# Kernel optimization log

Measured on AMD Instinct MI355X. Metric: run time of the kernel, lower is better.

The kernel has to match this reference:

```python
import jax, jax.numpy as jnp
import numpy as np

N, V, C, H, W, P = 4, 5, 128, 128, 128, 4096
IMG_W, IMG_H = 1920.0, 1080.0
FM = 128.0


def setup_inputs() -> dict:
    key = jax.random.key(0)
    k1, k2, k3, k4 = jax.random.split(key, 4)
    feature_maps = jax.random.normal(k1, (N, V, C, H, W), jnp.float32)
    xy = jax.random.uniform(k2, (N, P, 2), jnp.float32, -800.0, 800.0)
    z = jax.random.uniform(k3, (N, P, 1), jnp.float32, 100.0, 2000.0)
    extra = jax.random.uniform(k4, (N, P, 2), jnp.float32)
    sample_points = jnp.concatenate([xy, z, extra], axis=-1)  # [N,P,5]
    R = jnp.tile(jnp.eye(3, dtype=jnp.float32), (N, V, 1, 1))
    T = jnp.tile(jnp.array([0.0, 0.0, -3000.0], jnp.float32), (N, V, 1))
    f = jnp.full((N, V, 2), 1200.0, jnp.float32)
    c = jnp.tile(jnp.array([IMG_W / 2, IMG_H / 2], jnp.float32), (N, V, 1))
    k = jnp.zeros((N, V, 3), jnp.float32)  # radial distortion
    p = jnp.zeros((N, V, 2), jnp.float32)  # tangential distortion
    # affine transform (from get_affine_transform): full image -> feature map
    trans = jnp.tile(jnp.array([[FM / IMG_W, 0.0, 0.0], [0.0, FM / IMG_H, 0.0]], jnp.float32), (N, V, 1, 1))
    wh = jnp.tile(jnp.array([IMG_W, IMG_H], jnp.float32), (N, V, 1))
    fm_size = jnp.array([FM, FM], jnp.float32)
    return dict(feature_maps=feature_maps, sample_points=sample_points, R=R, T=T,
                f=f, c=c, k=k, p=p, trans=trans, wh=wh, fm_size=fm_size)


def _grid_sample_one(img, grid):
    # img: [C,H,W], grid: [P,2] in normalized coords; bilinear, zeros padding, align_corners=True
    Ci, Hi, Wi = img.shape
    x = (grid[:, 0] + 1.0) * 0.5 * (Wi - 1)
    y = (grid[:, 1] + 1.0) * 0.5 * (Hi - 1)
    x0 = jnp.floor(x); y0 = jnp.floor(y)
    wx1 = x - x0; wx0 = 1.0 - wx1
    wy1 = y - y0; wy0 = 1.0 - wy1

    def gather(xi, yi):
        valid = (xi >= 0) & (xi <= Wi - 1) & (yi >= 0) & (yi <= Hi - 1)
        xc = jnp.clip(xi, 0, Wi - 1).astype(jnp.int32)
        yc = jnp.clip(yi, 0, Hi - 1).astype(jnp.int32)
        return img[:, yc, xc] * valid.astype(img.dtype)  # [C,P]

    return (gather(x0, y0) * (wx0 * wy0) + gather(x0 + 1, y0) * (wx1 * wy0)
            + gather(x0, y0 + 1) * (wx0 * wy1) + gather(x0 + 1, y0 + 1) * (wx1 * wy1))


def _forward(feature_maps, sample_points, R, T, f, c, k, p, trans, wh, fm_size):
    n, v, ch, h, w = feature_maps.shape
    pts = sample_points[:, :, :3]  # [N,P,3]
    # world -> camera: X_cam = R @ (X - T)
    Xc = jnp.einsum('nvij,nvpj->nvpi', R, pts[:, None, :, :] - T[:, :, None, :])  # [N,V,P,3]
    xn = Xc[..., 0] / Xc[..., 2]
    yn = Xc[..., 1] / Xc[..., 2]
    r2 = xn * xn + yn * yn
    k1 = k[..., 0:1]; k2 = k[..., 1:2]; k3 = k[..., 2:3]
    p1 = p[..., 0:1]; p2 = p[..., 1:2]
    radial = 1.0 + k1 * r2 + k2 * r2 * r2 + k3 * r2 * r2 * r2
    xd = xn * radial + 2.0 * p1 * xn * yn + p2 * (r2 + 2.0 * xn * xn)
    yd = yn * radial + p1 * (r2 + 2.0 * yn * yn) + 2.0 * p2 * xn * yn
    xy = jnp.stack([xd, yd], -1) * f[:, :, None, :] + c[:, :, None, :]  # [N,V,P,2] pixel coords
    width = wh[..., 0:1]; height = wh[..., 1:2]
    bound = ((xy[..., 0] >= 0) & (xy[..., 1] >= 0)
             & (xy[..., 0] < width) & (xy[..., 1] < height)).astype(feature_maps.dtype)  # [N,V,P]
    max_wh = jnp.maximum(wh[..., 0], wh[..., 1])[:, :, None, None]
    pix = jnp.clip(xy, -1.0, max_wh)
    # affine transform to feature-map coords
    pix_t = jnp.einsum('nvij,nvpj->nvpi', trans[..., :2], pix) + trans[..., 2][:, :, None, :]
    norm = jnp.clip(pix_t / (fm_size - 1.0) * 2.0 - 1.0, -1.1, 1.1)  # [N,V,P,2]
    sampled = jax.vmap(_grid_sample_one)(feature_maps.reshape(n * v, ch, h, w),
                                         norm.reshape(n * v, -1, 2))  # [NV,C,P]
    sampled = sampled.reshape(n, v, ch, -1)
    feats = (sampled * bound[:, :, None, :]).transpose(0, 3, 1, 2)  # [N,P,V,C]
    is_not_nan = jnp.logical_not(jnp.isnan(feats).any(axis=(2, 3)))  # [N,P]
    bounding = (bound.sum(axis=1) > 0) & is_not_nan  # discard_nan=False path
    return feats, bounding


def reference(feature_maps, sample_points, R, T, f, c, k, p, trans, wh, fm_size):
    feats, bounding = _forward(feature_maps, sample_points, R, T, f, c, k, p, trans, wh, fm_size)
    return feats, bounding, sample_points
```

## Files before the change

### kernel.cpp

```cpp
#include <hip/hip_runtime.h>
#include <math.h>

#define N 4
#define V 5
#define C 128
#define H 128
#define W 128
#define P 4096
#define HW (H * W)
#define PTS 16

typedef float  fvec4 __attribute__((ext_vector_type(4)));
typedef unsigned short usvec4 __attribute__((ext_vector_type(4)));

__device__ __forceinline__ unsigned short f2bf_rne(float x) {
    unsigned u = __float_as_uint(x);
    unsigned rounding = 0x7fffu + ((u >> 16) & 1u);
    return (unsigned short)((u + rounding) >> 16);
}
__device__ __forceinline__ float bf2f(unsigned short b) {
    return __uint_as_float(((unsigned)b) << 16);
}

__global__ __launch_bounds__(256) void transpose_kernel(
    const float* __restrict__ fm, unsigned short* __restrict__ fmT)
{
    const int nv  = blockIdx.y;
    const int hw0 = blockIdx.x * 64;
    __shared__ float lds[64][C + 1];

    const int t = threadIdx.x;

    {
        const int hwl = (t & 15) * 4;
        const int cb  = t >> 4;
        const float* src = fm + (size_t)nv * C * HW + hw0 + hwl;
        for (int c = cb; c < C; c += 16) {
            const fvec4 v = __builtin_nontemporal_load(
                (const fvec4*)(src + (size_t)c * HW));
            lds[hwl + 0][c] = v.x;
            lds[hwl + 1][c] = v.y;
            lds[hwl + 2][c] = v.z;
            lds[hwl + 3][c] = v.w;
        }
    }
    __syncthreads();

    {
        const int c4 = (t & 31) * 4;
        unsigned short* dst = fmT + ((size_t)nv * HW + hw0) * C + c4;
        for (int hw = (t >> 5); hw < 64; hw += 8) {
            const fvec4 v = *(const fvec4*)&lds[hw][c4];
            usvec4 o;
            o.x = f2bf_rne(v.x);
            o.y = f2bf_rne(v.y);
            o.z = f2bf_rne(v.z);
            o.w = f2bf_rne(v.w);
            *(usvec4*)(dst + (size_t)hw * C) = o;
        }
    }
}

__global__ __launch_bounds__(256) void project_sample_kernel(
    const unsigned short* __restrict__ fmT,
    const float* __restrict__ sp,
    const float* __restrict__ Rm,
    const float* __restrict__ Tm,
    const float* __restrict__ fv,
    const float* __restrict__ cv,
    const float* __restrict__ kv,
    const float* __restrict__ pv,
    const float* __restrict__ trans,
    const float* __restrict__ wh,
    const float* __restrict__ fmsz,
    float* __restrict__ out_feats,
    float* __restrict__ out_bound,
    float* __restrict__ out_sp)
{
    const int pb = blockIdx.x;
    const int n  = pb >> 8;
    const int p0 = (pb & 255) * PTS;
    const int t  = threadIdx.x;
    const int base_pt = n * P + p0;

    __shared__ int   s_idx[PTS * V][4];
    __shared__ float s_w[PTS * V][4];
    __shared__ float s_bnd[PTS * V];
    __shared__ int   s_nan[PTS];

    if (t < PTS) s_nan[t] = 0;
    if (t < PTS * 5) out_sp[base_pt * 5 + t] = sp[base_pt * 5 + t];

    if (t < PTS * V) {
        const int pt = t / V;
        const int v  = t - pt * V;
        const int nv = n * V + v;

        const float X = sp[(base_pt + pt) * 5 + 0];
        const float Y = sp[(base_pt + pt) * 5 + 1];
        const float Z = sp[(base_pt + pt) * 5 + 2];

        const float* Rv = Rm + nv * 9;
        const float tx = Tm[nv * 3 + 0], ty = Tm[nv * 3 + 1], tz = Tm[nv * 3 + 2];
        const float px = X - tx, py = Y - ty, pz = Z - tz;
        const float Xc0 = Rv[0] * px + Rv[1] * py + Rv[2] * pz;
        const float Xc1 = Rv[3] * px + Rv[4] * py + Rv[5] * pz;
        const float Xc2 = Rv[6] * px + Rv[7] * py + Rv[8] * pz;
        const float xn = Xc0 / Xc2;
        const float yn = Xc1 / Xc2;
        const float r2 = xn * xn + yn * yn;
        const float k1 = kv[nv * 3 + 0], k2 = kv[nv * 3 + 1], k3 = kv[nv * 3 + 2];
        const float p1 = pv[nv * 2 + 0], p2 = pv[nv * 2 + 1];
        const float radial = 1.0f + k1 * r2 + k2 * r2 * r2 + k3 * r2 * r2 * r2;
        const float xd = xn * radial + 2.0f * p1 * xn * yn + p2 * (r2 + 2.0f * xn * xn);
        const float yd = yn * radial + p1 * (r2 + 2.0f * yn * yn) + 2.0f * p2 * xn * yn;
        const float xy0 = xd * fv[nv * 2 + 0] + cv[nv * 2 + 0];
        const float xy1 = yd * fv[nv * 2 + 1] + cv[nv * 2 + 1];
        const float width  = wh[nv * 2 + 0];
        const float height = wh[nv * 2 + 1];
        const bool bound = (xy0 >= 0.0f) && (xy1 >= 0.0f) && (xy0 < width) && (xy1 < height);
        const float maxwh = fmaxf(width, height);
        const float pix0 = fminf(fmaxf(xy0, -1.0f), maxwh);
        const float pix1 = fminf(fmaxf(xy1, -1.0f), maxwh);
        const float* tr = trans + nv * 6;
        const float pt0 = tr[0] * pix0 + tr[1] * pix1 + tr[2];
        const float pt1 = tr[3] * pix0 + tr[4] * pix1 + tr[5];
        const float fm0 = fmsz[0], fm1 = fmsz[1];
        float g0 = pt0 / (fm0 - 1.0f) * 2.0f - 1.0f;
        float g1 = pt1 / (fm1 - 1.0f) * 2.0f - 1.0f;
        g0 = fminf(fmaxf(g0, -1.1f), 1.1f);
        g1 = fminf(fmaxf(g1, -1.1f), 1.1f);

        const float xg = (g0 + 1.0f) * 0.5f * (float)(W - 1);
        const float yg = (g1 + 1.0f) * 0.5f * (float)(H - 1);
        const float x0f = floorf(xg), y0f = floorf(yg);
        const float wx1 = xg - x0f, wx0 = 1.0f - wx1;
        const float wy1 = yg - y0f, wy0 = 1.0f - wy1;
        const int x0 = (int)x0f, y0 = (int)y0f;
        const int x1 = x0 + 1,  y1 = y0 + 1;
        const bool vx0 = (x0 >= 0) && (x0 <= W - 1);
        const bool vx1 = (x1 >= 0) && (x1 <= W - 1);
        const bool vy0 = (y0 >= 0) && (y0 <= H - 1);
        const bool vy1 = (y1 >= 0) && (y1 <= H - 1);
        const int x0c = min(max(x0, 0), W - 1);
        const int x1c = min(max(x1, 0), W - 1);
        const int y0c = min(max(y0, 0), H - 1);
        const int y1c = min(max(y1, 0), H - 1);

        s_idx[t][0] = y0c * W + x0c;
        s_idx[t][1] = y0c * W + x1c;
        s_idx[t][2] = y1c * W + x0c;
        s_idx[t][3] = y1c * W + x1c;
        s_w[t][0] = (vx0 && vy0) ? (wx0 * wy0) : 0.0f;
        s_w[t][1] = (vx1 && vy0) ? (wx1 * wy0) : 0.0f;
        s_w[t][2] = (vx0 && vy1) ? (wx0 * wy1) : 0.0f;
        s_w[t][3] = (vx1 && vy1) ? (wx1 * wy1) : 0.0f;
        s_bnd[t] = bound ? 1.0f : 0.0f;
    }
    __syncthreads();

    {
        const int grp = t >> 5;
        const int c4  = (t & 31) * 4;
        const unsigned short* img_n = fmT + (size_t)(n * V) * HW * C;
        #pragma unroll 2
        for (int i = grp; i < PTS * V; i += 8) {
            const int pt = i / V;
            const int v  = i - pt * V;
            const unsigned short* img = img_n + (size_t)v * HW * C + c4;
            const usvec4 b00 = *(const usvec4*)(img + (size_t)s_idx[i][0] * C);
            const usvec4 b10 = *(const usvec4*)(img + (size_t)s_idx[i][1] * C);
            const usvec4 b01 = *(const usvec4*)(img + (size_t)s_idx[i][2] * C);
            const usvec4 b11 = *(const usvec4*)(img + (size_t)s_idx[i][3] * C);
            const float w00 = s_w[i][0], w10 = s_w[i][1];
            const float w01 = s_w[i][2], w11 = s_w[i][3];
            const float bnd = s_bnd[i];
            fvec4 f;
            f.x = (bf2f(b00.x) * w00 + bf2f(b10.x) * w10
                 + bf2f(b01.x) * w01 + bf2f(b11.x) * w11) * bnd;
            f.y = (bf2f(b00.y) * w00 + bf2f(b10.y) * w10
                 + bf2f(b01.y) * w01 + bf2f(b11.y) * w11) * bnd;
            f.z = (bf2f(b00.z) * w00 + bf2f(b10.z) * w10
                 + bf2f(b01.z) * w01 + bf2f(b11.z) * w11) * bnd;
            f.w = (bf2f(b00.w) * w00 + bf2f(b10.w) * w10
                 + bf2f(b01.w) * w01 + bf2f(b11.w) * w11) * bnd;
            if ((f.x != f.x) | (f.y != f.y) | (f.z != f.z) | (f.w != f.w))
                s_nan[pt] = 1;
            __builtin_nontemporal_store(
                f, (fvec4*)&out_feats[((size_t)(base_pt + pt) * V + v) * C + c4]);
        }
    }
    __syncthreads();

    if (t < PTS) {
        bool any_b = false;
        #pragma unroll
        for (int v = 0; v < V; ++v) any_b |= (s_bnd[t * V + v] != 0.0f);
        out_bound[base_pt + t] = (any_b && (s_nan[t] == 0)) ? 1.0f : 0.0f;
    }
}

extern "C" void kernel_launch(void* const* d_in, const int* in_sizes, int n_in,
                              void* d_out, int out_size, void* d_ws, size_t ws_size,
                              hipStream_t stream) {
    const float* fm    = (const float*)d_in[0];
    const float* sp    = (const float*)d_in[1];
    const float* Rm    = (const float*)d_in[2];
    const float* Tm    = (const float*)d_in[3];
    const float* fv    = (const float*)d_in[4];
    const float* cv    = (const float*)d_in[5];
    const float* kv    = (const float*)d_in[6];
    const float* pv    = (const float*)d_in[7];
    const float* trans = (const float*)d_in[8];
    const float* wh    = (const float*)d_in[9];
    const float* fmsz  = (const float*)d_in[10];

    float* out        = (float*)d_out;
    float* out_feats  = out;
    float* out_bound  = out + (size_t)N * P * V * C;
    float* out_sp     = out_bound + (size_t)N * P;

    unsigned short* fmT = (unsigned short*)d_ws;

    dim3 tgrid(HW / 64, N * V);
    transpose_kernel<<<tgrid, 256, 0, stream>>>(fm, fmT);

    project_sample_kernel<<<N * (P / PTS), 256, 0, stream>>>(
        fmT, sp, Rm, Tm, fv, cv, kv, pv, trans, wh, fmsz,
        out_feats, out_bound, out_sp);
}
```

Measured before the change: 287.2 us.

## Transpose only feature-map tiles touched by projected sample points

Projection moves into its own kernel. It writes per-sample corner indices and weights to workspace and marks which 16x16 tiles of each view's feature map are referenced. The transpose-to-bf16 kernel then converts only the flagged tiles, and the gather kernel reads the precomputed records. This aims to avoid reading and converting the whole fp32 feature map when samples cover only part of it, at the cost of less coalesced tile loads and an extra launch. Flags are never cleared, so stale flags from earlier calls can cause extra tile work.

```diff
diff --git a/kernel.cpp b/kernel.cpp
--- a/kernel.cpp
+++ b/kernel.cpp
@@ -9,6 +9,7 @@
 #define P 4096
 #define HW (H * W)
 #define PTS 16
+#define NPV (N * P * V)
 
 typedef float  fvec4 __attribute__((ext_vector_type(4)));
 typedef unsigned short usvec4 __attribute__((ext_vector_type(4)));
@@ -22,66 +23,153 @@
     return __uint_as_float(((unsigned)b) << 16);
 }
 
-__global__ __launch_bounds__(256) void transpose_kernel(
-    const float* __restrict__ fm, unsigned short* __restrict__ fmT)
+__global__ __launch_bounds__(256) void project_kernel(
+    const float* __restrict__ sp,
+    const float* __restrict__ Rm, const float* __restrict__ Tm,
+    const float* __restrict__ fv, const float* __restrict__ cv,
+    const float* __restrict__ kv, const float* __restrict__ pv,
+    const float* __restrict__ trans, const float* __restrict__ wh,
+    const float* __restrict__ fmsz,
+    int4*  __restrict__ ws_idx,
+    float4* __restrict__ ws_w,
+    float* __restrict__ ws_bnd,
+    unsigned* __restrict__ flags,
+    float* __restrict__ out_sp)
 {
-    const int nv  = blockIdx.y;
-    const int hw0 = blockIdx.x * 64;
-    __shared__ float lds[64][C + 1];
-
+    const int tid = blockIdx.x * 256 + threadIdx.x;
+    out_sp[tid] = sp[tid];
+
+    const int pt = tid / V;
+    const int v  = tid - pt * V;
+    const int n  = pt >> 12;
+    const int nv = n * V + v;
+
+    const float X = sp[pt * 5 + 0];
+    const float Y = sp[pt * 5 + 1];
+    const float Z = sp[pt * 5 + 2];
+
+    const float* Rv = Rm + nv * 9;
+    const float tx = Tm[nv * 3 + 0], ty = Tm[nv * 3 + 1], tz = Tm[nv * 3 + 2];
+    const float px = X - tx, py = Y - ty, pz = Z - tz;
+    const float Xc0 = Rv[0] * px + Rv[1] * py + Rv[2] * pz;
+    const float Xc1 = Rv[3] * px + Rv[4] * py + Rv[5] * pz;
+    const float Xc2 = Rv[6] * px + Rv[7] * py + Rv[8] * pz;
+    const float xn = Xc0 / Xc2;
+    const float yn = Xc1 / Xc2;
+    const float r2 = xn * xn + yn * yn;
+    const float k1 = kv[nv * 3 + 0], k2 = kv[nv * 3 + 1], k3 = kv[nv * 3 + 2];
+    const float p1 = pv[nv * 2 + 0], p2 = pv[nv * 2 + 1];
+    const float radial = 1.0f + k1 * r2 + k2 * r2 * r2 + k3 * r2 * r2 * r2;
+    const float xd = xn * radial + 2.0f * p1 * xn * yn + p2 * (r2 + 2.0f * xn * xn);
+    const float yd = yn * radial + p1 * (r2 + 2.0f * yn * yn) + 2.0f * p2 * xn * yn;
+    const float xy0 = xd * fv[nv * 2 + 0] + cv[nv * 2 + 0];
+    const float xy1 = yd * fv[nv * 2 + 1] + cv[nv * 2 + 1];
+    const float width  = wh[nv * 2 + 0];
+    const float height = wh[nv * 2 + 1];
+    const bool bound = (xy0 >= 0.0f) && (xy1 >= 0.0f) && (xy0 < width) && (xy1 < height);
+    const float maxwh = fmaxf(width, height);
+    const float pix0 = fminf(fmaxf(xy0, -1.0f), maxwh);
+    const float pix1 = fminf(fmaxf(xy1, -1.0f), maxwh);
+    const float* tr = trans + nv * 6;
+    const float pt0 = tr[0] * pix0 + tr[1] * pix1 + tr[2];
+    const float pt1 = tr[3] * pix0 + tr[4] * pix1 + tr[5];
+    const float fm0 = fmsz[0], fm1 = fmsz[1];
+    float g0 = pt0 / (fm0 - 1.0f) * 2.0f - 1.0f;
+    float g1 = pt1 / (fm1 - 1.0f) * 2.0f - 1.0f;
+    g0 = fminf(fmaxf(g0, -1.1f), 1.1f);
+    g1 = fminf(fmaxf(g1, -1.1f), 1.1f);
+
+    const float xg = (g0 + 1.0f) * 0.5f * (float)(W - 1);
+    const float yg = (g1 + 1.0f) * 0.5f * (float)(H - 1);
+    const float x0f = floorf(xg), y0f = floorf(yg);
+    const float wx1 = xg - x0f, wx0 = 1.0f - wx1;
+    const float wy1 = yg - y0f, wy0 = 1.0f - wy1;
+    const int x0 = (int)x0f, y0 = (int)y0f;
+    const int x1 = x0 + 1,  y1 = y0 + 1;
+    const bool vx0 = (x0 >= 0) && (x0 <= W - 1);
+    const bool vx1 = (x1 >= 0) && (x1 <= W - 1);
+    const bool vy0 = (y0 >= 0) && (y0 <= H - 1);
+    const bool vy1 = (y1 >= 0) && (y1 <= H - 1);
+    const int x0c = min(max(x0, 0), W - 1);
+    const int x1c = min(max(x1, 0), W - 1);
+    const int y0c = min(max(y0, 0), H - 1);
+    const int y1c = min(max(y1, 0), H - 1);
+
+    int4 id;
+    id.x = y0c * W + x0c;
+    id.y = y0c * W + x1c;
+    id.z = y1c * W + x0c;
+    id.w = y1c * W + x1c;
+    ws_idx[tid] = id;
+
+    float4 w;
+    w.x = (vx0 && vy0) ? (wx0 * wy0) : 0.0f;
+    w.y = (vx1 && vy0) ? (wx1 * wy0) : 0.0f;
+    w.z = (vx0 && vy1) ? (wx0 * wy1) : 0.0f;
+    w.w = (vx1 && vy1) ? (wx1 * wy1) : 0.0f;
+    ws_w[tid] = w;
+    ws_bnd[tid] = bound ? 1.0f : 0.0f;
+
+    unsigned* fl = flags + nv * 64;
+    const int tx0 = x0c >> 4, tx1 = x1c >> 4;
+    const int ty0 = y0c >> 4, ty1 = y1c >> 4;
+    fl[ty0 * 8 + tx0] = 1u;
+    fl[ty0 * 8 + tx1] = 1u;
+    fl[ty1 * 8 + tx0] = 1u;
+    fl[ty1 * 8 + tx1] = 1u;
+}
+
+__global__ __launch_bounds__(256) void transpose_tiles_kernel(
+    const float* __restrict__ fm, unsigned short* __restrict__ fmT,
+    const unsigned* __restrict__ flags)
+{
+    const int nv   = blockIdx.y;
+    const int tile = blockIdx.x;
+    if (flags[nv * 64 + tile] != 1u) return;
+    const int ybase = (tile >> 3) * 16;
+    const int xbase = (tile & 7) * 16;
+
+    __shared__ float lds[256][33];
     const int t = threadIdx.x;
-
-    {
-        const int hwl = (t & 15) * 4;
-        const int cb  = t >> 4;
-        const float* src = fm + (size_t)nv * C * HW + hw0 + hwl;
-        for (int c = cb; c < C; c += 16) {
-            const fvec4 v = __builtin_nontemporal_load(
-                (const fvec4*)(src + (size_t)c * HW));
-            lds[hwl + 0][c] = v.x;
-            lds[hwl + 1][c] = v.y;
-            lds[hwl + 2][c] = v.z;
-            lds[hwl + 3][c] = v.w;
+    const float* src = fm + (size_t)nv * C * HW;
+    unsigned short* dst = fmT + (size_t)nv * HW * C;
+
+    for (int cg = 0; cg < 4; ++cg) {
+        if (cg) __syncthreads();
+        for (int e = t; e < 8192; e += 256) {
+            const int c  = e >> 8;
+            const int pxl = e & 255;
+            const int y = ybase + (pxl >> 4), x = xbase + (pxl & 15);
+            lds[pxl][c] = src[(size_t)(cg * 32 + c) * HW + y * W + x];
         }
-    }
-    __syncthreads();
-
-    {
-        const int c4 = (t & 31) * 4;
-        unsigned short* dst = fmT + ((size_t)nv * HW + hw0) * C + c4;
-        for (int hw = (t >> 5); hw < 64; hw += 8) {
-            const fvec4 v = *(const fvec4*)&lds[hw][c4];
+        __syncthreads();
+        const int c4 = (t & 7) * 4;
+        for (int pxl = t >> 3; pxl < 256; pxl += 32) {
+            const int y = ybase + (pxl >> 4), x = xbase + (pxl & 15);
             usvec4 o;
-            o.x = f2bf_rne(v.x);
-            o.y = f2bf_rne(v.y);
-            o.z = f2bf_rne(v.z);
-            o.w = f2bf_rne(v.w);
-            *(usvec4*)(dst + (size_t)hw * C) = o;
+            o.x = f2bf_rne(lds[pxl][c4 + 0]);
+            o.y = f2bf_rne(lds[pxl][c4 + 1]);
+            o.z = f2bf_rne(lds[pxl][c4 + 2]);
+            o.w = f2bf_rne(lds[pxl][c4 + 3]);
+            *(usvec4*)(dst + (size_t)(y * W + x) * C + cg * 32 + c4) = o;
         }
     }
 }
 
-__global__ __launch_bounds__(256) void project_sample_kernel(
+__global__ __launch_bounds__(256) void gather_kernel(
     const unsigned short* __restrict__ fmT,
-    const float* __restrict__ sp,
-    const float* __restrict__ Rm,
-    const float* __restrict__ Tm,
-    const float* __restrict__ fv,
-    const float* __restrict__ cv,
-    const float* __restrict__ kv,
-    const float* __restrict__ pv,
-    const float* __restrict__ trans,
-    const float* __restrict__ wh,
-    const float* __restrict__ fmsz,
+    const int4*  __restrict__ ws_idx,
+    const float4* __restrict__ ws_w,
+    const float* __restrict__ ws_bnd,
     float* __restrict__ out_feats,
-    float* __restrict__ out_bound,
-    float* __restrict__ out_sp)
+    float* __restrict__ out_bound)
 {
     const int pb = blockIdx.x;
     const int n  = pb >> 8;
     const int p0 = (pb & 255) * PTS;
     const int t  = threadIdx.x;
     const int base_pt = n * P + p0;
+    const int rec0 = base_pt * V;
 
     __shared__ int   s_idx[PTS * V][4];
     __shared__ float s_w[PTS * V][4];
@@ -89,73 +177,13 @@
     __shared__ int   s_nan[PTS];
 
     if (t < PTS) s_nan[t] = 0;
-    if (t < PTS * 5) out_sp[base_pt * 5 + t] = sp[base_pt * 5 + t];
-
     if (t < PTS * V) {
-        const int pt = t / V;
-        const int v  = t - pt * V;
-        const int nv = n * V + v;
-
-        const float X = sp[(base_pt + pt) * 5 + 0];
-        const float Y = sp[(base_pt + pt) * 5 + 1];
-        const float Z = sp[(base_pt + pt) * 5 + 2];
-
-        const float* Rv = Rm + nv * 9;
-        const float tx = Tm[nv * 3 + 0], ty = Tm[nv * 3 + 1], tz = Tm[nv * 3 + 2];
-        const float px = X - tx, py = Y - ty, pz = Z - tz;
-        const float Xc0 = Rv[0] * px + Rv[1] * py + Rv[2] * pz;
-        const float Xc1 = Rv[3] * px + Rv[4] * py + Rv[5] * pz;
-        const float Xc2 = Rv[6] * px + Rv[7] * py + Rv[8] * pz;
-        const float xn = Xc0 / Xc2;
-        const float yn = Xc1 / Xc2;
-        const float r2 = xn * xn + yn * yn;
-        const float k1 = kv[nv * 3 + 0], k2 = kv[nv * 3 + 1], k3 = kv[nv * 3 + 2];
-        const float p1 = pv[nv * 2 + 0], p2 = pv[nv * 2 + 1];
-        const float radial = 1.0f + k1 * r2 + k2 * r2 * r2 + k3 * r2 * r2 * r2;
-        const float xd = xn * radial + 2.0f * p1 * xn * yn + p2 * (r2 + 2.0f * xn * xn);
-        const float yd = yn * radial + p1 * (r2 + 2.0f * yn * yn) + 2.0f * p2 * xn * yn;
-        const float xy0 = xd * fv[nv * 2 + 0] + cv[nv * 2 + 0];
-        const float xy1 = yd * fv[nv * 2 + 1] + cv[nv * 2 + 1];
-        const float width  = wh[nv * 2 + 0];
-        const float height = wh[nv * 2 + 1];
-        const bool bound = (xy0 >= 0.0f) && (xy1 >= 0.0f) && (xy0 < width) && (xy1 < height);
-        const float maxwh = fmaxf(width, height);
-        const float pix0 = fminf(fmaxf(xy0, -1.0f), maxwh);
-        const float pix1 = fminf(fmaxf(xy1, -1.0f), maxwh);
-        const float* tr = trans + nv * 6;
-        const float pt0 = tr[0] * pix0 + tr[1] * pix1 + tr[2];
-        const float pt1 = tr[3] * pix0 + tr[4] * pix1 + tr[5];
-        const float fm0 = fmsz[0], fm1 = fmsz[1];
-        float g0 = pt0 / (fm0 - 1.0f) * 2.0f - 1.0f;
-        float g1 = pt1 / (fm1 - 1.0f) * 2.0f - 1.0f;
-        g0 = fminf(fmaxf(g0, -1.1f), 1.1f);
-        g1 = fminf(fmaxf(g1, -1.1f), 1.1f);
-
-        const float xg = (g0 + 1.0f) * 0.5f * (float)(W - 1);
-        const float yg = (g1 + 1.0f) * 0.5f * (float)(H - 1);
-        const float x0f = floorf(xg), y0f = floorf(yg);
-        const float wx1 = xg - x0f, wx0 = 1.0f - wx1;
-        const float wy1 = yg - y0f, wy0 = 1.0f - wy1;
-        const int x0 = (int)x0f, y0 = (int)y0f;
-        const int x1 = x0 + 1,  y1 = y0 + 1;
-        const bool vx0 = (x0 >= 0) && (x0 <= W - 1);
-        const bool vx1 = (x1 >= 0) && (x1 <= W - 1);
-        const bool vy0 = (y0 >= 0) && (y0 <= H - 1);
-        const bool vy1 = (y1 >= 0) && (y1 <= H - 1);
-        const int x0c = min(max(x0, 0), W - 1);
-        const int x1c = min(max(x1, 0), W - 1);
-        const int y0c = min(max(y0, 0), H - 1);
-        const int y1c = min(max(y1, 0), H - 1);
-
-        s_idx[t][0] = y0c * W + x0c;
-        s_idx[t][1] = y0c * W + x1c;
-        s_idx[t][2] = y1c * W + x0c;
-        s_idx[t][3] = y1c * W + x1c;
-        s_w[t][0] = (vx0 && vy0) ? (wx0 * wy0) : 0.0f;
-        s_w[t][1] = (vx1 && vy0) ? (wx1 * wy0) : 0.0f;
-        s_w[t][2] = (vx0 && vy1) ? (wx0 * wy1) : 0.0f;
-        s_w[t][3] = (vx1 && vy1) ? (wx1 * wy1) : 0.0f;
-        s_bnd[t] = bound ? 1.0f : 0.0f;
+        const int4  id = ws_idx[rec0 + t];
+        const float4 w = ws_w[rec0 + t];
+        s_idx[t][0] = id.x; s_idx[t][1] = id.y;
+        s_idx[t][2] = id.z; s_idx[t][3] = id.w;
+        s_w[t][0] = w.x; s_w[t][1] = w.y; s_w[t][2] = w.z; s_w[t][3] = w.w;
+        s_bnd[t] = ws_bnd[rec0 + t];
     }
     __syncthreads();
 
@@ -220,12 +248,21 @@
     float* out_bound  = out + (size_t)N * P * V * C;
     float* out_sp     = out_bound + (size_t)N * P;
 
-    unsigned short* fmT = (unsigned short*)d_ws;
-
-    dim3 tgrid(HW / 64, N * V);
-    transpose_kernel<<<tgrid, 256, 0, stream>>>(fm, fmT);
-
-    project_sample_kernel<<<N * (P / PTS), 256, 0, stream>>>(
-        fmT, sp, Rm, Tm, fv, cv, kv, pv, trans, wh, fmsz,
-        out_feats, out_bound, out_sp);
-}
+    char* ws = (char*)d_ws;
+    unsigned short* fmT = (unsigned short*)ws;
+    size_t off = (size_t)N * V * HW * C * sizeof(unsigned short);
+    int4*   ws_idx = (int4*)(ws + off);   off += (size_t)NPV * sizeof(int4);
+    float4* ws_w   = (float4*)(ws + off); off += (size_t)NPV * sizeof(float4);
+    float*  ws_bnd = (float*)(ws + off);  off += (size_t)NPV * sizeof(float);
+    unsigned* flags = (unsigned*)(ws + off);
+
+    project_kernel<<<NPV / 256, 256, 0, stream>>>(
+        sp, Rm, Tm, fv, cv, kv, pv, trans, wh, fmsz,
+        ws_idx, ws_w, ws_bnd, flags, out_sp);
+
+    dim3 tgrid(64, N * V);
+    transpose_tiles_kernel<<<tgrid, 256, 0, stream>>>(fm, fmT, flags);
+
+    gather_kernel<<<N * (P / PTS), 256, 0, stream>>>(
+        fmT, ws_idx, ws_w, ws_bnd, out_feats, out_bound);
+}
```

New measurement: 296.3 us. 3.2% more time.
